# Optimization experiments

Hardware: AMD Instinct MI355X
Metric: run time of the kernel (lower is better)

Reference implementation:

```python
import jax, jax.numpy as jnp
import numpy as np

D_MODEL = 1024
NHEAD = 16
DFF = 4096
B = 4
L = 1024
EPS = 1e-5


def _layernorm(x, g, b):
    mu = jnp.mean(x, axis=-1, keepdims=True)
    var = jnp.mean((x - mu) ** 2, axis=-1, keepdims=True)
    return (x - mu) * jax.lax.rsqrt(var + EPS) * g + b


def _mha(q, k, v, wq, bq, wk, bk, wv, bv, wo, bo, mask=None):
    # q: [B,Lq,D], k/v: [B,Lk,D]; weights stored as [D_in, D_out]
    Bq, Lq, D = q.shape
    depth = D // NHEAD

    def split(x):  # [B,L,D] -> [B,H,L,depth]
        return x.reshape(Bq, -1, NHEAD, depth).transpose(0, 2, 1, 3)

    Q = split(q @ wq + bq)
    K = split(k @ wk + bk)
    V = split(v @ wv + bv)
    logits = jnp.einsum('bhqd,bhkd->bhqk', Q, K) / (depth ** 0.5)
    if mask is not None:
        logits = jnp.where(mask, logits, jnp.asarray(-1e9, logits.dtype))
    w = jax.nn.softmax(logits, axis=-1)
    o = jnp.einsum('bhqk,bhkd->bhqd', w, V)
    o = o.transpose(0, 2, 1, 3).reshape(Bq, -1, D)
    return o @ wo + bo


def setup_inputs() -> dict:
    key = jax.random.key(0)
    ks = jax.random.split(key, 16)
    s = 0.02

    def w(k, shp):
        return jax.random.normal(k, shp, jnp.float32) * s

    d, f = D_MODEL, DFF
    inp = {
        'tgt': jax.random.normal(ks[0], (B, L, d), jnp.float32),
        'memory': jax.random.normal(ks[1], (B, L, d), jnp.float32),
        'tgt_mask': jnp.tril(jnp.ones((L, L), jnp.bool_)),
        # self-attention params
        'sa_wq': w(ks[2], (d, d)), 'sa_bq': jnp.zeros((d,), jnp.float32),
        'sa_wk': w(ks[3], (d, d)), 'sa_bk': jnp.zeros((d,), jnp.float32),
        'sa_wv': w(ks[4], (d, d)), 'sa_bv': jnp.zeros((d,), jnp.float32),
        'sa_wo': w(ks[5], (d, d)), 'sa_bo': jnp.zeros((d,), jnp.float32),
        # cross-attention params
        'ca_wq': w(ks[6], (d, d)), 'ca_bq': jnp.zeros((d,), jnp.float32),
        'ca_wk': w(ks[7], (d, d)), 'ca_bk': jnp.zeros((d,), jnp.float32),
        'ca_wv': w(ks[8], (d, d)), 'ca_bv': jnp.zeros((d,), jnp.float32),
        'ca_wo': w(ks[9], (d, d)), 'ca_bo': jnp.zeros((d,), jnp.float32),
        # FFN params
        'ffn_w1': w(ks[10], (d, f)), 'ffn_b1': jnp.zeros((f,), jnp.float32),
        'ffn_w2': w(ks[11], (f, d)), 'ffn_b2': jnp.zeros((d,), jnp.float32),
        # LayerNorm params
        'ln1_g': jnp.ones((d,), jnp.float32), 'ln1_b': jnp.zeros((d,), jnp.float32),
        'ln2_g': jnp.ones((d,), jnp.float32), 'ln2_b': jnp.zeros((d,), jnp.float32),
        'ln3_g': jnp.ones((d,), jnp.float32), 'ln3_b': jnp.zeros((d,), jnp.float32),
    }
    return inp


def reference(tgt, memory, tgt_mask,
              sa_wq, sa_bq, sa_wk, sa_bk, sa_wv, sa_bv, sa_wo, sa_bo,
              ca_wq, ca_bq, ca_wk, ca_bk, ca_wv, ca_bv, ca_wo, ca_bo,
              ffn_w1, ffn_b1, ffn_w2, ffn_b2,
              ln1_g, ln1_b, ln2_g, ln2_b, ln3_g, ln3_b):
    # merge_mask with key_padding_mask=None -> mask used directly, broadcast over B,H
    mask = tgt_mask[None, None, :, :]
    t2 = _mha(tgt, tgt, tgt, sa_wq, sa_bq, sa_wk, sa_bk, sa_wv, sa_bv, sa_wo, sa_bo, mask)
    x = _layernorm(tgt + t2, ln1_g, ln1_b)
    t2 = _mha(x, memory, memory, ca_wq, ca_bq, ca_wk, ca_bk, ca_wv, ca_bv, ca_wo, ca_bo, None)
    x = _layernorm(x + t2, ln2_g, ln2_b)
    t2 = jax.nn.relu(x @ ffn_w1 + ffn_b1) @ ffn_w2 + ffn_b2
    x = _layernorm(x + t2, ln3_g, ln3_b)
    return x
```

## Files before the change

### kernel.cpp

```cpp
#include <hip/hip_runtime.h>
#include <hip/hip_bf16.h>

typedef unsigned short u16;
typedef __attribute__((ext_vector_type(8))) short bf16x8;
typedef __attribute__((ext_vector_type(4))) float floatx4;

__device__ inline float u2f(unsigned u) { union { unsigned i; float f; } x; x.i = u; return x.f; }
__device__ inline float bflo(unsigned p) { return u2f(p << 16); }
__device__ inline float bfhi(unsigned p) { return u2f(p & 0xffff0000u); }
__device__ inline u16 f2bf(float f) {
    union { __hip_bfloat16 h; u16 u; } x;
    x.h = __float2bfloat16(f);
    return x.u;
}
__device__ inline unsigned pk2bf(float lo, float hi) {
    return ((unsigned)f2bf(hi) << 16) | f2bf(lo);
}

#define SCLQ 0.18033688011f

#define GLDS(g, l) __builtin_amdgcn_global_load_lds( \
    (const __attribute__((address_space(1))) void*)(g), \
    (__attribute__((address_space(3))) void*)(l), 16, 0, 0)

template<int EPI, int NF, int MW>
__global__ __launch_bounds__(256, (MW == 8) ? 2 : 3) void gemm_mfma(
        const u16* __restrict__ A, const u16* __restrict__ Bt,
        const float* __restrict__ bias, const u16* __restrict__ res,
        void* __restrict__ Cv, u16* __restrict__ o1, u16* __restrict__ o2,
        int N, int K)
{
    constexpr int BN = NF * 32;
    constexpr int BM = MW * 32;
    constexpr int MFR = BM / 32;
    constexpr int ALOADS = BM / 64;
    constexpr int BLOADS = BN / 64;
    constexpr int LOADS = ALOADS + BLOADS;

    __shared__ u16 As0[BM * 32];
    __shared__ u16 Bs0[BN * 32];
    __shared__ u16 As1[BM * 32];
    __shared__ u16 Bs1[BN * 32];
    __shared__ u16 As2[BM * 32];
    __shared__ u16 Bs2[BN * 32];

    const int tid = threadIdx.x;
    const int lane = tid & 63, wv = tid >> 6;
    const int wr = wv >> 1, wc = wv & 1;

    const int gx = gridDim.x;
    const int nwg = gx * gridDim.y;
    const int bid0 = blockIdx.y * gx + blockIdx.x;
    const int nbid = (bid0 & 7) * (nwg >> 3) + (bid0 >> 3);
    const int bx = nbid % gx, by = nbid / gx;
    const int row0 = by * BM, col0 = bx * BN;

    const int Keff = (EPI == 7) ? (K >> 1) : K;
    const int k0off = (EPI == 7) ? blockIdx.z * Keff : 0;

    const u16* pa[ALOADS];
    int ldst[ALOADS];
    #pragma unroll
    for (int i = 0; i < ALOADS; ++i) {
        const int idx = i * 256 + tid;
        const int r = idx >> 2;
        const int kob = (idx & 3) << 4;
        const int sw = kob ^ (((r >> 1) & 3) << 4);
        pa[i] = A + (size_t)(row0 + r) * K + k0off + (sw >> 1);
        ldst[i] = idx * 8;
    }
    const u16* pb[BLOADS];
    int ldstB[BLOADS];
    #pragma unroll
    for (int i = 0; i < BLOADS; ++i) {
        const int idx = i * 256 + tid;
        const int r = idx >> 2;
        const int kob = (idx & 3) << 4;
        const int sw = kob ^ (((r >> 1) & 3) << 4);
        pb[i] = Bt + (size_t)(col0 + r) * K + k0off + (sw >> 1);
        ldstB[i] = idx * 8;
    }

    int offa[MFR], offb[NF];
    const int rsel = lane & 15, slot = lane >> 4;
    #pragma unroll
    for (int m = 0; m < MFR; ++m) {
        const int ra = wr * (BM / 2) + m * 16 + rsel;
        offa[m] = ra * 32 + (((slot << 4) ^ (((ra >> 1) & 3) << 4)) >> 1);
    }
    #pragma unroll
    for (int n = 0; n < NF; ++n) {
        const int rb = wc * (NF * 16) + n * 16 + rsel;
        offb[n] = rb * 32 + (((slot << 4) ^ (((rb >> 1) & 3) << 4)) >> 1);
    }

    floatx4 acc[MFR][NF] = {};

#define STAGE(AA, BB, t) do {                                   \
        const int ko_ = (t) << 5;                               \
        _Pragma("unroll")                                       \
        for (int i = 0; i < ALOADS; ++i)                        \
            GLDS(pa[i] + ko_, &AA[ldst[i]]);                    \
        _Pragma("unroll")                                       \
        for (int i = 0; i < BLOADS; ++i)                        \
            GLDS(pb[i] + ko_, &BB[ldstB[i]]);                   \
    } while (0)

#define COMPUTE(AA, BB) do {                                    \
        bf16x8 af[MFR], bfr[NF];                                \
        _Pragma("unroll")                                       \
        for (int m = 0; m < MFR; ++m) af[m] = *(const bf16x8*)&AA[offa[m]]; \
        _Pragma("unroll")                                       \
        for (int n = 0; n < NF; ++n) bfr[n] = *(const bf16x8*)&BB[offb[n]]; \
        _Pragma("unroll")                                       \
        for (int m = 0; m < MFR; ++m)                           \
            _Pragma("unroll")                                   \
            for (int n = 0; n < NF; ++n)                        \
                acc[m][n] = __builtin_amdgcn_mfma_f32_16x16x32_bf16( \
                        af[m], bfr[n], acc[m][n], 0, 0, 0);     \
    } while (0)

#define PHASE(CA, CB, NA, NB, t) do {                           \
        if ((t) < nkt - 1) {                                    \
            if constexpr (LOADS == 6)                           \
                asm volatile("s_waitcnt vmcnt(6)" ::: "memory");\
            else if constexpr (LOADS == 4)                      \
                asm volatile("s_waitcnt vmcnt(4)" ::: "memory");\
            else                                                \
                asm volatile("s_waitcnt vmcnt(3)" ::: "memory");\
        } else {                                                \
            asm volatile("s_waitcnt vmcnt(0)" ::: "memory");    \
        }                                                       \
        __builtin_amdgcn_s_barrier();                           \
        __builtin_amdgcn_sched_barrier(0);                      \
        if ((t) + 2 < nkt) STAGE(NA, NB, (t) + 2);              \
        COMPUTE(CA, CB);                                        \
    } while (0)

    const int nkt = Keff >> 5;
    STAGE(As0, Bs0, 0);
    STAGE(As1, Bs1, 1);
    int t = 0;
    for (; t + 3 <= nkt; t += 3) {
        PHASE(As0, Bs0, As2, Bs2, t);
        PHASE(As1, Bs1, As0, Bs0, t + 1);
        PHASE(As2, Bs2, As1, Bs1, t + 2);
    }
    if (t < nkt)     PHASE(As0, Bs0, As2, Bs2, t);
    if (t + 1 < nkt) PHASE(As1, Bs1, As0, Bs0, t + 1);
#undef STAGE
#undef COMPUTE
#undef PHASE

    const int cr4 = (lane >> 4) * 4;
    const int cc = lane & 15;

    if (EPI == 7) {
        float* dst = (blockIdx.z == 0) ? (float*)Cv : (float*)o1;
        const bool addb = (blockIdx.z == 0);
        #pragma unroll
        for (int n = 0; n < NF; ++n) {
            const int col = col0 + wc * (NF * 16) + n * 16 + cc;
            const float bv = addb ? bias[col] : 0.f;
            #pragma unroll
            for (int m = 0; m < MFR; ++m) {
                const int rowb = row0 + wr * (BM / 2) + m * 16 + cr4;
                #pragma unroll
                for (int r = 0; r < 4; ++r)
                    dst[(size_t)(rowb + r) * N + col] = acc[m][n][r] + bv;
            }
        }
        return;
    }

    if (EPI == 5 || EPI == 6) {
        const int seg = col0 >> 10;
        const int vtseg = (EPI == 5) ? 2 : 1;
        u16* dst;
        if (EPI == 5) dst = (seg == 0) ? (u16*)Cv : (seg == 1 ? o1 : o2);
        else          dst = (seg == 0) ? (u16*)Cv : o1;

        if (seg == vtseg) {
            #pragma unroll
            for (int n = 0; n < NF; ++n) {
                const int col = col0 + wc * (NF * 16) + n * 16 + cc;
                const float bv = bias[col];
                const int vcol = col & 1023;
                const int h = vcol >> 6, d = vcol & 63;
                #pragma unroll
                for (int m = 0; m < MFR; ++m) {
                    const int tk = row0 + wr * (BM / 2) + m * 16 + cr4;
                    const int b = tk >> 10;
                    ushort4 o4;
                    o4.x = f2bf(acc[m][n][0] + bv);
                    o4.y = f2bf(acc[m][n][1] + bv);
                    o4.z = f2bf(acc[m][n][2] + bv);
                    o4.w = f2bf(acc[m][n][3] + bv);
                    *(ushort4*)(dst +
                        (((size_t)(b * 16 + h) * 64 + d) * 1024 + (tk & 1023))) = o4;
                }
            }
        } else {
            const float osc = (EPI == 5 && seg == 0) ? SCLQ : 1.f;
            #pragma unroll
            for (int n = 0; n < NF; ++n) {
                const int col = col0 + wc * (NF * 16) + n * 16 + cc;
                const float bv = bias[col];
                const int oc = col & 1023;
                #pragma unroll
                for (int m = 0; m < MFR; ++m) {
                    const int rowb = row0 + wr * (BM / 2) + m * 16 + cr4;
                    #pragma unroll
                    for (int r = 0; r < 4; ++r)
                        dst[(size_t)(rowb + r) * 1024 + oc] = f2bf((acc[m][n][r] + bv) * osc);
                }
            }
        }
        return;
    }

    #pragma unroll
    for (int n = 0; n < NF; ++n) {
        const int col = col0 + wc * (NF * 16) + n * 16 + cc;
        const float bv = bias[col];
        #pragma unroll
        for (int m = 0; m < MFR; ++m) {
            const int rowb = row0 + wr * (BM / 2) + m * 16 + cr4;
            #pragma unroll
            for (int r = 0; r < 4; ++r) {
                float v = acc[m][n][r] + bv;
                const size_t o = (size_t)(rowb + r) * N + col;
                if (EPI == 2) v += u2f((unsigned)res[o] << 16);
                if (EPI == 1) v = fmaxf(v, 0.f);
                if (EPI == 8) v *= SCLQ;
                ((u16*)Cv)[o] = f2bf(v);
            }
        }
    }
}

struct PrepArgs {
    const float* w[10];
    u16* o[10];
    const float* tgt; const float* mem;
    u16* tgtb; u16* memb;
    const float* bq; const float* bk; const float* bv;
    const float* cbk; const float* cbv;
    float* biasQKV; float* biasKV;
};

__global__ __launch_bounds__(256) void prep_kernel(PrepArgs p)
{
    __shared__ float ts[64][65];
    const int tid = threadIdx.x;
    int bid = blockIdx.x;

    if (bid < 4096) {
        int w, n0, k0, K, N;
        if (bid < 2048) {
            w = bid >> 8;
            const int t = bid & 255;
            n0 = (t & 15) * 64; k0 = ((t >> 4) & 15) * 64; K = 1024; N = 1024;
        } else if (bid < 3072) {
            w = 8;
            const int t = bid - 2048;
            n0 = (t & 63) * 64; k0 = (t >> 6) * 64; K = 1024; N = 4096;
        } else {
            w = 9;
            const int t = bid - 3072;
            n0 = (t & 15) * 64; k0 = (t >> 4) * 64; K = 4096; N = 1024;
        }
        const float* __restrict__ W = p.w[w];
        u16* __restrict__ Wt = p.o[w];
        const int tr = tid >> 4, tc4 = (tid & 15) * 4;
        #pragma unroll
        for (int i = 0; i < 4; ++i) {
            const float4 v = *(const float4*)(W + (size_t)(k0 + tr + i * 16) * N + n0 + tc4);
            ts[tr + i * 16][tc4 + 0] = v.x;
            ts[tr + i * 16][tc4 + 1] = v.y;
            ts[tr + i * 16][tc4 + 2] = v.z;
            ts[tr + i * 16][tc4 + 3] = v.w;
        }
        __syncthreads();
        #pragma unroll
        for (int i = 0; i < 4; ++i) {
            const int nr = tr + i * 16;
            ushort4 o;
            o.x = f2bf(ts[tc4 + 0][nr]);
            o.y = f2bf(ts[tc4 + 1][nr]);
            o.z = f2bf(ts[tc4 + 2][nr]);
            o.w = f2bf(ts[tc4 + 3][nr]);
            *(ushort4*)(Wt + (size_t)(n0 + nr) * K + k0 + tc4) = o;
        }
        return;
    }
    bid -= 4096;
    if (bid < 4096) {
        const int i = bid * 256 + tid;
        const float4 v = ((const float4*)p.tgt)[i];
        ushort4 o;
        o.x = f2bf(v.x); o.y = f2bf(v.y); o.z = f2bf(v.z); o.w = f2bf(v.w);
        ((ushort4*)p.tgtb)[i] = o;
        return;
    }
    bid -= 4096;
    if (bid < 4096) {
        const int i = bid * 256 + tid;
        const float4 v = ((const float4*)p.mem)[i];
        ushort4 o;
        o.x = f2bf(v.x); o.y = f2bf(v.y); o.z = f2bf(v.z); o.w = f2bf(v.w);
        ((ushort4*)p.memb)[i] = o;
        return;
    }
    bid -= 4096;
    const int i = bid * 256 + tid;
    if (i < 3072)
        p.biasQKV[i] = (i < 1024) ? p.bq[i] : (i < 2048 ? p.bk[i - 1024] : p.bv[i - 2048]);
    if (i < 2048)
        p.biasKV[i] = (i < 1024) ? p.cbk[i] : p.cbv[i - 1024];
}

template<int CAUSAL>
__global__ __launch_bounds__(256) void fattn_mfma(
        const u16* __restrict__ Q, const u16* __restrict__ K,
        const u16* __restrict__ Vt, u16* __restrict__ O)
{
    __shared__ u16 Ks[64 * 64];
    __shared__ u16 Vs[64 * 64];
    __shared__ u16 Ps[64 * 64];

    const int tid = threadIdx.x;
    const int lane = tid & 63, wv = tid >> 6;
    const int g = lane >> 4, qx = lane & 15;
    const int bh = blockIdx.x;
    const int b = bh >> 4, h = bh & 15;
    const int qt = blockIdx.y, q0 = qt * 64;

    const size_t qkbase = (size_t)b * (1024 * 1024) + (size_t)h * 64;
    const size_t vtbase = (size_t)bh * 64 * 1024;

    const int qr = wv * 16 + qx;
    const int qg = q0 + qr;
    const int swzq = (qr & 7) << 4;

    bf16x8 qf[2];
    #pragma unroll
    for (int ks = 0; ks < 2; ++ks)
        qf[ks] = *(const bf16x8*)(Q + qkbase + (size_t)qg * 1024 + ks * 32 + g * 8);

    const int r0 = tid >> 3, s0 = tid & 7;

    float l_i = 0.f;
    floatx4 o_acc[4] = {};

    const int ktmax = CAUSAL ? qt : 15;
    for (int kt = 0; kt <= ktmax; ++kt) {
        __syncthreads();
        #pragma unroll
        for (int i = 0; i < 2; ++i) {
            const int r = i * 32 + r0;
            const uint4 kv = *(const uint4*)(K + qkbase + (size_t)(kt * 64 + r) * 1024 + s0 * 8);
            *(uint4*)((char*)Ks + r * 128 + ((s0 ^ (r & 7)) << 4)) = kv;
            const uint4 vv = *(const uint4*)(Vt + vtbase + (size_t)r * 1024 + kt * 64 + s0 * 8);
            *(uint4*)((char*)Vs + r * 128 + ((s0 ^ (r & 7)) << 4)) = vv;
        }
        __syncthreads();

        floatx4 sa[4] = {};
        #pragma unroll
        for (int ks = 0; ks < 2; ++ks) {
            #pragma unroll
            for (int m = 0; m < 4; ++m) {
                const int rr = m * 16 + qx;
                const int sl = ks * 4 + g;
                const bf16x8 kf = *(const bf16x8*)((char*)Ks + rr * 128 + ((sl ^ (rr & 7)) << 4));
                sa[m] = __builtin_amdgcn_mfma_f32_16x16x32_bf16(kf, qf[ks], sa[m], 0, 0, 0);
            }
        }

        float p[4][4];
        float rs = 0.f;
        #pragma unroll
        for (int m = 0; m < 4; ++m)
            #pragma unroll
            for (int r = 0; r < 4; ++r) {
                float e = exp2f(sa[m][r]);
                if (CAUSAL && kt == qt) {
                    const int kl = m * 16 + g * 4 + r;
                    if (kl > qr) e = 0.f;
                }
                p[m][r] = e;
                rs += e;
            }
        rs += __shfl_xor(rs, 16);
        rs += __shfl_xor(rs, 32);
        l_i += rs;

        #pragma unroll
        for (int m = 0; m < 4; ++m) {
            uint2 pk;
            pk.x = pk2bf(p[m][0], p[m][1]);
            pk.y = pk2bf(p[m][2], p[m][3]);
            *(uint2*)((char*)Ps + qr * 128 + ((m * 32 + g * 8) ^ swzq)) = pk;
        }

        #pragma unroll
        for (int ks2 = 0; ks2 < 2; ++ks2) {
            const bf16x8 pf = *(const bf16x8*)((char*)Ps + qr * 128 + ((ks2 * 64 + g * 16) ^ swzq));
            #pragma unroll
            for (int n = 0; n < 4; ++n) {
                const int rv = n * 16 + qx;
                const int sl = ks2 * 4 + g;
                const bf16x8 vf = *(const bf16x8*)((char*)Vs + rv * 128 + ((sl ^ (rv & 7)) << 4));
                o_acc[n] = __builtin_amdgcn_mfma_f32_16x16x32_bf16(vf, pf, o_acc[n], 0, 0, 0);
            }
        }
    }

    const float inv = 1.f / l_i;
    #pragma unroll
    for (int n = 0; n < 4; ++n) {
        uint2 ov;
        ov.x = pk2bf(o_acc[n][0] * inv, o_acc[n][1] * inv);
        ov.y = pk2bf(o_acc[n][2] * inv, o_acc[n][3] * inv);
        *(uint2*)((char*)Ps + qr * 128 + ((n * 32 + g * 8) ^ swzq)) = ov;
    }
    const int orow = wv * 16 + (lane >> 2);
    const int swzo = (orow & 7) << 4;
    #pragma unroll
    for (int i = 0; i < 2; ++i) {
        const int cb = ((lane & 3) * 2 + i) * 16;
        const uint4 ov = *(const uint4*)((char*)Ps + orow * 128 + (cb ^ swzo));
        *(uint4*)(O + qkbase + (size_t)(q0 + orow) * 1024 + cb / 2) = ov;
    }
}

__global__ __launch_bounds__(256) void ln_bf16_kernel(
        const u16* __restrict__ X, const float* __restrict__ g,
        const float* __restrict__ bta, u16* __restrict__ Y)
{
    __shared__ float red[4];
    const int row = blockIdx.x, tid = threadIdx.x;
    const int wave = tid >> 6, lane = tid & 63;

    const uint2 u = *(const uint2*)(X + (size_t)row * 1024 + tid * 4);
    const float x0 = bflo(u.x), x1 = bfhi(u.x), x2 = bflo(u.y), x3 = bfhi(u.y);

    float s = x0 + x1 + x2 + x3;
    #pragma unroll
    for (int off = 32; off; off >>= 1) s += __shfl_xor(s, off);
    if (lane == 0) red[wave] = s;
    __syncthreads();
    const float mu = (red[0] + red[1] + red[2] + red[3]) * (1.f / 1024.f);
    __syncthreads();

    const float d0 = x0 - mu, d1 = x1 - mu, d2 = x2 - mu, d3 = x3 - mu;
    float s2 = d0 * d0 + d1 * d1 + d2 * d2 + d3 * d3;
    #pragma unroll
    for (int off = 32; off; off >>= 1) s2 += __shfl_xor(s2, off);
    if (lane == 0) red[wave] = s2;
    __syncthreads();
    const float var = (red[0] + red[1] + red[2] + red[3]) * (1.f / 1024.f);
    const float rs = rsqrtf(var + 1e-5f);

    const float4 gg = ((const float4*)g)[tid];
    const float4 bb = ((const float4*)bta)[tid];
    ushort4 o;
    o.x = f2bf(d0 * rs * gg.x + bb.x);
    o.y = f2bf(d1 * rs * gg.y + bb.y);
    o.z = f2bf(d2 * rs * gg.z + bb.z);
    o.w = f2bf(d3 * rs * gg.w + bb.w);
    *(ushort4*)(Y + (size_t)row * 1024 + tid * 4) = o;
}

__global__ __launch_bounds__(256) void ln_res_kernel(
        const float* X0, const float* __restrict__ X1,
        const u16* __restrict__ res, const float* __restrict__ g,
        const float* __restrict__ bta, float* Y)
{
    __shared__ float red[4];
    const int row = blockIdx.x;
    const int tid = threadIdx.x;
    const int wave = tid >> 6, lane = tid & 63;

    const float4 v0 = ((const float4*)(X0 + (size_t)row * 1024))[tid];
    const float4 v1 = ((const float4*)(X1 + (size_t)row * 1024))[tid];
    const uint2 u = *(const uint2*)(res + (size_t)row * 1024 + tid * 4);
    const float x0 = v0.x + v1.x + bflo(u.x), x1 = v0.y + v1.y + bfhi(u.x);
    const float x2 = v0.z + v1.z + bflo(u.y), x3 = v0.w + v1.w + bfhi(u.y);

    float s = x0 + x1 + x2 + x3;
    #pragma unroll
    for (int off = 32; off; off >>= 1) s += __shfl_xor(s, off);
    if (lane == 0) red[wave] = s;
    __syncthreads();
    const float mu = (red[0] + red[1] + red[2] + red[3]) * (1.f / 1024.f);
    __syncthreads();

    const float d0 = x0 - mu, d1 = x1 - mu, d2 = x2 - mu, d3 = x3 - mu;
    float s2 = d0 * d0 + d1 * d1 + d2 * d2 + d3 * d3;
    #pragma unroll
    for (int off = 32; off; off >>= 1) s2 += __shfl_xor(s2, off);
    if (lane == 0) red[wave] = s2;
    __syncthreads();
    const float var = (red[0] + red[1] + red[2] + red[3]) * (1.f / 1024.f);
    const float rs = rsqrtf(var + 1e-5f);

    const float4 gg = ((const float4*)g)[tid];
    const float4 bb = ((const float4*)bta)[tid];
    float4 o;
    o.x = d0 * rs * gg.x + bb.x;
    o.y = d1 * rs * gg.y + bb.y;
    o.z = d2 * rs * gg.z + bb.z;
    o.w = d3 * rs * gg.w + bb.w;
    ((float4*)(Y + (size_t)row * 1024))[tid] = o;
}

extern "C" void kernel_launch(void* const* d_in, const int* in_sizes, int n_in,
                              void* d_out, int out_size, void* d_ws, size_t ws_size,
                              hipStream_t stream)
{
    const float* tgt    = (const float*)d_in[0];
    const float* mem    = (const float*)d_in[1];
    const float* sa_wq  = (const float*)d_in[3];
    const float* sa_bq  = (const float*)d_in[4];
    const float* sa_wk  = (const float*)d_in[5];
    const float* sa_bk  = (const float*)d_in[6];
    const float* sa_wv  = (const float*)d_in[7];
    const float* sa_bv  = (const float*)d_in[8];
    const float* sa_wo  = (const float*)d_in[9];
    const float* sa_bo  = (const float*)d_in[10];
    const float* ca_wq  = (const float*)d_in[11];
    const float* ca_bq  = (const float*)d_in[12];
    const float* ca_wk  = (const float*)d_in[13];
    const float* ca_bk  = (const float*)d_in[14];
    const float* ca_wv  = (const float*)d_in[15];
    const float* ca_bv  = (const float*)d_in[16];
    const float* ca_wo  = (const float*)d_in[17];
    const float* ca_bo  = (const float*)d_in[18];
    const float* ffn_w1 = (const float*)d_in[19];
    const float* ffn_b1 = (const float*)d_in[20];
    const float* ffn_w2 = (const float*)d_in[21];
    const float* ffn_b2 = (const float*)d_in[22];
    const float* ln1_g  = (const float*)d_in[23];
    const float* ln1_b  = (const float*)d_in[24];
    const float* ln2_g  = (const float*)d_in[25];
    const float* ln2_b  = (const float*)d_in[26];
    const float* ln3_g  = (const float*)d_in[27];
    const float* ln3_b  = (const float*)d_in[28];

    float* out = (float*)d_out;
    u16* wsb = (u16*)d_ws;
    const size_t M1 = 1024 * 1024;

    u16* Wsq = wsb + 0 * M1;
    u16* Wsk = wsb + 1 * M1;
    u16* Wsv = wsb + 2 * M1;
    u16* Wso = wsb + 3 * M1;
    u16* Wcq = wsb + 4 * M1;
    u16* Wck = wsb + 5 * M1;
    u16* Wcv = wsb + 6 * M1;
    u16* Wco = wsb + 7 * M1;
    u16* Wf1 = wsb + 8 * M1;
    u16* Wf2 = wsb + 12 * M1;

    u16* sl = wsb + 16 * M1;
    u16* s0 = sl + 0 * 4 * M1;
    u16* s1 = sl + 4 * M1;
    u16* s2 = sl + 8 * M1;
    u16* s3 = sl + 12 * M1;
    u16* s4 = sl + 16 * M1;
    u16* s5 = sl + 20 * M1;
    u16* H  = s0;

    float* part1 = (float*)wsb;

    float* biasQKV = (float*)(wsb + 40 * M1);
    float* biasKV  = biasQKV + 3072;

    const dim3 blk(256);
    const dim3 gqkv(24, 32);
    const dim3 gkv(16, 32);
    const dim3 g1(16, 32);
    const dim3 g4(32, 16);
    const dim3 gf2(8, 32, 2);
    const dim3 ga(64, 16);
    const dim3 gln(4096);

    PrepArgs pa;
    pa.w[0] = sa_wq; pa.o[0] = Wsq;
    pa.w[1] = sa_wk; pa.o[1] = Wsk;
    pa.w[2] = sa_wv; pa.o[2] = Wsv;
    pa.w[3] = sa_wo; pa.o[3] = Wso;
    pa.w[4] = ca_wq; pa.o[4] = Wcq;
    pa.w[5] = ca_wk; pa.o[5] = Wck;
    pa.w[6] = ca_wv; pa.o[6] = Wcv;
    pa.w[7] = ca_wo; pa.o[7] = Wco;
    pa.w[8] = ffn_w1; pa.o[8] = Wf1;
    pa.w[9] = ffn_w2; pa.o[9] = Wf2;
    pa.tgt = tgt; pa.mem = mem; pa.tgtb = s0; pa.memb = s1;
    pa.bq = sa_bq; pa.bk = sa_bk; pa.bv = sa_bv;
    pa.cbk = ca_bk; pa.cbv = ca_bv;
    pa.biasQKV = biasQKV; pa.biasKV = biasKV;
    prep_kernel<<<12308, blk, 0, stream>>>(pa);

    gemm_mfma<5, 4, 4><<<gqkv, blk, 0, stream>>>(s0, Wsq, biasQKV, nullptr,
                                                 s2, s3, s4, 3072, 1024);
    fattn_mfma<1><<<ga, blk, 0, stream>>>(s2, s3, s4, s5);
    gemm_mfma<2, 2, 4><<<g1, blk, 0, stream>>>(s5, Wso, sa_bo, s0, s2, nullptr, nullptr, 1024, 1024);
    ln_bf16_kernel<<<gln, blk, 0, stream>>>(s2, ln1_g, ln1_b, s3);

    gemm_mfma<8, 2, 4><<<g1, blk, 0, stream>>>(s3, Wcq, ca_bq, nullptr, s2, nullptr, nullptr, 1024, 1024);
    gemm_mfma<6, 4, 4><<<gkv, blk, 0, stream>>>(s1, Wck, biasKV, nullptr,
                                                s4, s5, nullptr, 2048, 1024);
    fattn_mfma<0><<<ga, blk, 0, stream>>>(s2, s4, s5, s0);
    gemm_mfma<2, 2, 4><<<g1, blk, 0, stream>>>(s0, Wco, ca_bo, s3, s2, nullptr, nullptr, 1024, 1024);
    ln_bf16_kernel<<<gln, blk, 0, stream>>>(s2, ln2_g, ln2_b, s4);

    gemm_mfma<1, 4, 8><<<g4, blk, 0, stream>>>(s4, Wf1, ffn_b1, nullptr, H, nullptr, nullptr, 4096, 1024);
    gemm_mfma<7, 4, 4><<<gf2, blk, 0, stream>>>(H, Wf2, ffn_b2, nullptr, out,
                                                (u16*)part1, nullptr, 1024, 4096);
    ln_res_kernel<<<gln, blk, 0, stream>>>(out, part1, s4, ln3_g, ln3_b, out);
}
```

Before: 318.0 us.

## Process two adjacent query tiles per attention block to reuse K/V tiles

```diff
diff --git a/kernel.cpp b/kernel.cpp
--- a/kernel.cpp
+++ b/kernel.cpp
@@ -327,34 +327,39 @@
 {
     __shared__ u16 Ks[64 * 64];
     __shared__ u16 Vs[64 * 64];
-    __shared__ u16 Ps[64 * 64];
+    __shared__ u16 PsA[64 * 64];
+    __shared__ u16 PsB[64 * 64];
 
     const int tid = threadIdx.x;
     const int lane = tid & 63, wv = tid >> 6;
     const int g = lane >> 4, qx = lane & 15;
     const int bh = blockIdx.x;
     const int b = bh >> 4, h = bh & 15;
-    const int qt = blockIdx.y, q0 = qt * 64;
+    const int jt = blockIdx.y;
+    const int tiA = 2 * jt, tiB = 2 * jt + 1;
+    const int q0A = tiA * 64, q0B = tiB * 64;
 
     const size_t qkbase = (size_t)b * (1024 * 1024) + (size_t)h * 64;
     const size_t vtbase = (size_t)bh * 64 * 1024;
 
     const int qr = wv * 16 + qx;
-    const int qg = q0 + qr;
     const int swzq = (qr & 7) << 4;
 
-    bf16x8 qf[2];
-    #pragma unroll
-    for (int ks = 0; ks < 2; ++ks)
-        qf[ks] = *(const bf16x8*)(Q + qkbase + (size_t)qg * 1024 + ks * 32 + g * 8);
+    bf16x8 qfA[2], qfB[2];
+    #pragma unroll
+    for (int ks = 0; ks < 2; ++ks) {
+        qfA[ks] = *(const bf16x8*)(Q + qkbase + (size_t)(q0A + qr) * 1024 + ks * 32 + g * 8);
+        qfB[ks] = *(const bf16x8*)(Q + qkbase + (size_t)(q0B + qr) * 1024 + ks * 32 + g * 8);
+    }
 
     const int r0 = tid >> 3, s0 = tid & 7;
 
-    float l_i = 0.f;
-    floatx4 o_acc[4] = {};
-
-    const int ktmax = CAUSAL ? qt : 15;
+    float lA = 0.f, lB = 0.f;
+    floatx4 oA[4] = {}, oB[4] = {};
+
+    const int ktmax = CAUSAL ? tiB : 15;
     for (int kt = 0; kt <= ktmax; ++kt) {
+        const bool doA = !CAUSAL || (kt <= tiA);
         __syncthreads();
         #pragma unroll
         for (int i = 0; i < 2; ++i) {
@@ -366,7 +371,7 @@
         }
         __syncthreads();
 
-        floatx4 sa[4] = {};
+        floatx4 saA[4] = {}, saB[4] = {};
         #pragma unroll
         for (int ks = 0; ks < 2; ++ks) {
             #pragma unroll
@@ -374,64 +379,107 @@
                 const int rr = m * 16 + qx;
                 const int sl = ks * 4 + g;
                 const bf16x8 kf = *(const bf16x8*)((char*)Ks + rr * 128 + ((sl ^ (rr & 7)) << 4));
-                sa[m] = __builtin_amdgcn_mfma_f32_16x16x32_bf16(kf, qf[ks], sa[m], 0, 0, 0);
-            }
-        }
-
-        float p[4][4];
-        float rs = 0.f;
-        #pragma unroll
-        for (int m = 0; m < 4; ++m)
-            #pragma unroll
-            for (int r = 0; r < 4; ++r) {
-                float e = exp2f(sa[m][r]);
-                if (CAUSAL && kt == qt) {
-                    const int kl = m * 16 + g * 4 + r;
-                    if (kl > qr) e = 0.f;
+                if (doA)
+                    saA[m] = __builtin_amdgcn_mfma_f32_16x16x32_bf16(kf, qfA[ks], saA[m], 0, 0, 0);
+                saB[m] = __builtin_amdgcn_mfma_f32_16x16x32_bf16(kf, qfB[ks], saB[m], 0, 0, 0);
+            }
+        }
+
+        if (doA) {
+            float rs = 0.f;
+            float p[4][4];
+            #pragma unroll
+            for (int m = 0; m < 4; ++m)
+                #pragma unroll
+                for (int r = 0; r < 4; ++r) {
+                    float e = exp2f(saA[m][r]);
+                    if (CAUSAL && kt == tiA) {
+                        const int kl = m * 16 + g * 4 + r;
+                        if (kl > qr) e = 0.f;
+                    }
+                    p[m][r] = e;
+                    rs += e;
                 }
-                p[m][r] = e;
-                rs += e;
-            }
-        rs += __shfl_xor(rs, 16);
-        rs += __shfl_xor(rs, 32);
-        l_i += rs;
-
-        #pragma unroll
-        for (int m = 0; m < 4; ++m) {
-            uint2 pk;
-            pk.x = pk2bf(p[m][0], p[m][1]);
-            pk.y = pk2bf(p[m][2], p[m][3]);
-            *(uint2*)((char*)Ps + qr * 128 + ((m * 32 + g * 8) ^ swzq)) = pk;
+            rs += __shfl_xor(rs, 16);
+            rs += __shfl_xor(rs, 32);
+            lA += rs;
+            #pragma unroll
+            for (int m = 0; m < 4; ++m) {
+                uint2 pk;
+                pk.x = pk2bf(p[m][0], p[m][1]);
+                pk.y = pk2bf(p[m][2], p[m][3]);
+                *(uint2*)((char*)PsA + qr * 128 + ((m * 32 + g * 8) ^ swzq)) = pk;
+            }
+        }
+        {
+            float rs = 0.f;
+            float p[4][4];
+            #pragma unroll
+            for (int m = 0; m < 4; ++m)
+                #pragma unroll
+                for (int r = 0; r < 4; ++r) {
+                    float e = exp2f(saB[m][r]);
+                    if (CAUSAL && kt == tiB) {
+                        const int kl = m * 16 + g * 4 + r;
+                        if (kl > qr) e = 0.f;
+                    }
+                    p[m][r] = e;
+                    rs += e;
+                }
+            rs += __shfl_xor(rs, 16);
+            rs += __shfl_xor(rs, 32);
+            lB += rs;
+            #pragma unroll
+            for (int m = 0; m < 4; ++m) {
+                uint2 pk;
+                pk.x = pk2bf(p[m][0], p[m][1]);
+                pk.y = pk2bf(p[m][2], p[m][3]);
+                *(uint2*)((char*)PsB + qr * 128 + ((m * 32 + g * 8) ^ swzq)) = pk;
+            }
         }
 
         #pragma unroll
         for (int ks2 = 0; ks2 < 2; ++ks2) {
-            const bf16x8 pf = *(const bf16x8*)((char*)Ps + qr * 128 + ((ks2 * 64 + g * 16) ^ swzq));
+            bf16x8 vf[4];
             #pragma unroll
             for (int n = 0; n < 4; ++n) {
                 const int rv = n * 16 + qx;
                 const int sl = ks2 * 4 + g;
-                const bf16x8 vf = *(const bf16x8*)((char*)Vs + rv * 128 + ((sl ^ (rv & 7)) << 4));
-                o_acc[n] = __builtin_amdgcn_mfma_f32_16x16x32_bf16(vf, pf, o_acc[n], 0, 0, 0);
-            }
-        }
-    }
-
-    const float inv = 1.f / l_i;
+                vf[n] = *(const bf16x8*)((char*)Vs + rv * 128 + ((sl ^ (rv & 7)) << 4));
+            }
+            if (doA) {
+                const bf16x8 pfA = *(const bf16x8*)((char*)PsA + qr * 128 + ((ks2 * 64 + g * 16) ^ swzq));
+                #pragma unroll
+                for (int n = 0; n < 4; ++n)
+                    oA[n] = __builtin_amdgcn_mfma_f32_16x16x32_bf16(vf[n], pfA, oA[n], 0, 0, 0);
+            }
+            const bf16x8 pfB = *(const bf16x8*)((char*)PsB + qr * 128 + ((ks2 * 64 + g * 16) ^ swzq));
+            #pragma unroll
+            for (int n = 0; n < 4; ++n)
+                oB[n] = __builtin_amdgcn_mfma_f32_16x16x32_bf16(vf[n], pfB, oB[n], 0, 0, 0);
+        }
+    }
+
+    const float invA = 1.f / lA, invB = 1.f / lB;
     #pragma unroll
     for (int n = 0; n < 4; ++n) {
-        uint2 ov;
-        ov.x = pk2bf(o_acc[n][0] * inv, o_acc[n][1] * inv);
-        ov.y = pk2bf(o_acc[n][2] * inv, o_acc[n][3] * inv);
-        *(uint2*)((char*)Ps + qr * 128 + ((n * 32 + g * 8) ^ swzq)) = ov;
+        uint2 ovA, ovB;
+        ovA.x = pk2bf(oA[n][0] * invA, oA[n][1] * invA);
+        ovA.y = pk2bf(oA[n][2] * invA, oA[n][3] * invA);
+        *(uint2*)((char*)PsA + qr * 128 + ((n * 32 + g * 8) ^ swzq)) = ovA;
+        ovB.x = pk2bf(oB[n][0] * invB, oB[n][1] * invB);
+        ovB.y = pk2bf(oB[n][2] * invB, oB[n][3] * invB);
+        *(uint2*)((char*)PsB + qr * 128 + ((n * 32 + g * 8) ^ swzq)) = ovB;
     }
     const int orow = wv * 16 + (lane >> 2);
     const int swzo = (orow & 7) << 4;
     #pragma unroll
     for (int i = 0; i < 2; ++i) {
         const int cb = ((lane & 3) * 2 + i) * 16;
-        const uint4 ov = *(const uint4*)((char*)Ps + orow * 128 + (cb ^ swzo));
-        *(uint4*)(O + qkbase + (size_t)(q0 + orow) * 1024 + cb / 2) = ov;
+        const uint4 ovA = *(const uint4*)((char*)PsA + orow * 128 + (cb ^ swzo));
+        *(uint4*)(O + qkbase + (size_t)(q0A + orow) * 1024 + cb / 2) = ovA;
+        const uint4 ovB = *(const uint4*)((char*)PsB + orow * 128 + (cb ^ swzo));
+        *(uint4*)(O + qkbase + (size_t)(q0B + orow) * 1024 + cb / 2) = ovB;
     }
 }
 
@@ -584,7 +632,7 @@
     const dim3 g1(16, 32);
     const dim3 g4(32, 16);
     const dim3 gf2(8, 32, 2);
-    const dim3 ga(64, 16);
+    const dim3 ga(64, 8);
     const dim3 gln(4096);
 
     PrepArgs pa;
```

New measurement: 336.3 us. 1.06x slower.
